# Kernel optimization log

Hardware: AMD Instinct MI355X
Metric: run time of the kernel (lower is better)

## Reference

```python
import jax, jax.numpy as jnp
import numpy as np

N_NODES = 10000
N_EDGES = 160000
NEG_SLOPE = 0.2


def setup_inputs() -> dict:
    key = jax.random.key(0)
    ks = jax.random.split(key, 24)

    def rn(k, shape, scale):
        return (jax.random.normal(k, shape, dtype=jnp.float32) * scale)

    inp = {
        "x": rn(ks[0], (N_NODES, 128), 1.0),
        "edge_index": jax.random.randint(ks[1], (2, N_EDGES), 0, N_NODES, dtype=jnp.int32),
        "edge_attr": rn(ks[2], (N_EDGES, 8), 1.0),
        # GATConv 1: 128 -> 64 (heads=1)
        "W1": rn(ks[3], (128, 64), 0.09), "as1": rn(ks[4], (64,), 0.1), "ad1": rn(ks[5], (64,), 0.1), "b1": rn(ks[6], (64,), 0.01),
        # GATConv 2: 64 -> 256
        "W2": rn(ks[7], (64, 256), 0.125), "as2": rn(ks[8], (256,), 0.06), "ad2": rn(ks[9], (256,), 0.06), "b2": rn(ks[10], (256,), 0.01),
        # GATConv 3: 256 -> 1024
        "W3": rn(ks[11], (256, 1024), 0.0625), "as3": rn(ks[12], (1024,), 0.03), "ad3": rn(ks[13], (1024,), 0.03), "b3": rn(ks[14], (1024,), 0.01),
        # Dense head
        "lw1": rn(ks[15], (1024, 512), 0.03), "lb1": rn(ks[16], (512,), 0.01),
        "lw2": rn(ks[17], (512, 10), 0.04), "lb2": rn(ks[18], (10,), 0.01),
    }
    return inp


def gat_layer(x, src, dst, W, a_s, a_d, b, n):
    """PyG GATConv, heads=1, concat=True, add_self_loops handled by caller via src/dst."""
    h = x @ W                                   # [N, F_out]
    e = jax.nn.leaky_relu((h @ a_s)[src] + (h @ a_d)[dst], NEG_SLOPE)  # [E']
    m = jax.ops.segment_max(e, dst, num_segments=n)
    ex = jnp.exp(e - m[dst])
    denom = jax.ops.segment_sum(ex, dst, num_segments=n)
    alpha = ex / denom[dst]                     # scatter-softmax over incoming edges
    out = jax.ops.segment_sum(alpha[:, None] * h[src], dst, num_segments=n)
    return out + b


def reference(x, edge_index, edge_attr, W1, as1, ad1, b1, W2, as2, ad2, b2,
              W3, as3, ad3, b3, lw1, lb1, lw2, lb2):
    # edge_attr is accepted but ignored (GATConv built without edge_dim)
    n = x.shape[0]
    loops = jnp.arange(n, dtype=edge_index.dtype)  # add_self_loops=True
    src = jnp.concatenate([edge_index[0], loops])
    dst = jnp.concatenate([edge_index[1], loops])

    h = jax.nn.relu(gat_layer(x, src, dst, W1, as1, ad1, b1, n))
    h = jax.nn.relu(gat_layer(h, src, dst, W2, as2, ad2, b2, n))
    h = jax.nn.relu(gat_layer(h, src, dst, W3, as3, ad3, b3, n))

    pooled = jnp.max(h, axis=0, keepdims=True)  # global_max_pool, batch=None -> [1, 1024]
    z = jax.nn.relu(pooled @ lw1 + lb1)
    z = z @ lw2 + lb2
    return jax.nn.log_softmax(z, axis=1)
```

## Files before the change

kernel.cpp:

```cpp
#include <hip/hip_runtime.h>
#include <hip/hip_bf16.h>
#include <math.h>

#define NEG_SLOPE 0.2f
typedef unsigned short u16;
typedef short bf16x8 __attribute__((ext_vector_type(8)));
typedef float f32x4 __attribute__((ext_vector_type(4)));

__device__ __forceinline__ float bfu2f(u16 u) { return __uint_as_float(((unsigned)u) << 16); }
__device__ __forceinline__ u16 f2bu(float v) { return __bfloat16_as_ushort(__float2bfloat16(v)); }

__device__ __forceinline__ void gload_lds16(const void* g, void* l) {
    __builtin_amdgcn_global_load_lds((const __attribute__((address_space(1))) void*)g,
                                     (__attribute__((address_space(3))) void*)l, 16, 0, 0);
}

__global__ void prep_kernel(int* deg, int* cursor, float* pooled, int N,
                            const float* __restrict__ x, u16* __restrict__ xb,
                            const float* __restrict__ W1, u16* __restrict__ Wt1,
                            const float* __restrict__ W2, u16* __restrict__ Wt2,
                            const float* __restrict__ W3, u16* __restrict__ Wt3,
                            const float* __restrict__ as2, const float* __restrict__ ad2,
                            const float* __restrict__ as3, const float* __restrict__ ad3,
                            float* __restrict__ ws2, float* __restrict__ wd2,
                            float* __restrict__ ws3, float* __restrict__ wd3,
                            int c0, int c1, int c2, int c3, int c4) {
    int bid = blockIdx.x, tid = threadIdx.x;
    if (bid < c0) {
        int i = bid * 256 + tid;
        if (i < N) { deg[i] = 0; cursor[i] = 0; }
        if (i < 1024) pooled[i] = 0.f;
    } else if (bid < c1) {
        int i = (bid - c0) * 256 + tid;
        if (i < N * 128) xb[i] = f2bu(x[i]);
    } else if (bid < c2) {
        int i = (bid - c1) * 256 + tid;
        int k = i % 128, f = i / 128;
        Wt1[i] = f2bu(W1[k * 64 + f]);
    } else if (bid < c3) {
        int i = (bid - c2) * 256 + tid;
        int k = i % 64, f = i / 64;
        Wt2[i] = f2bu(W2[k * 256 + f]);
    } else if (bid < c4) {
        int i = (bid - c3) * 256 + tid;
        int k = i % 256, f = i / 256;
        Wt3[i] = f2bu(W3[(size_t)k * 1024 + f]);
    } else {
        int wv = ((bid - c4) * 256 + tid) >> 6;
        int lane = tid & 63;
        const float *W, *va, *vd; float *os, *od; int F, row;
        if (wv < 64) { W = W2; va = as2; vd = ad2; F = 256; row = wv; os = ws2; od = wd2; }
        else if (wv < 320) { W = W3; va = as3; vd = ad3; F = 1024; row = wv - 64; os = ws3; od = wd3; }
        else return;
        const float* wr = W + (size_t)row * F;
        float ss = 0.f, dd = 0.f;
        for (int f = lane; f < F; f += 64) { float wvv = wr[f]; ss += wvv * va[f]; dd += wvv * vd[f]; }
        for (int off = 32; off; off >>= 1) { ss += __shfl_xor(ss, off); dd += __shfl_xor(dd, off); }
        if (lane == 0) { os[row] = ss; od[row] = dd; }
    }
}

__global__ void count_kernel(const int* __restrict__ edst, int E, int N, int* deg) {
    int i = blockIdx.x * blockDim.x + threadIdx.x;
    int total = E + N;
    if (i >= total) return;
    int dn = (i < E) ? edst[i] : (i - E);
    atomicAdd(&deg[dn], 1);
}

__global__ void scan_kernel(const int* __restrict__ deg, int N, int* __restrict__ offsets) {
    __shared__ int part[257];
    int tid = threadIdx.x;
    int chunk = (N + 255) / 256;
    int begin = tid * chunk;
    int fin = begin + chunk; if (fin > N) fin = N; if (begin > N) begin = N;
    int sum = 0;
    for (int i = begin; i < fin; ++i) sum += deg[i];
    part[tid] = sum;
    __syncthreads();
    if (tid == 0) {
        int acc = 0;
        for (int t = 0; t < 256; ++t) { int v = part[t]; part[t] = acc; acc += v; }
        part[256] = acc;
    }
    __syncthreads();
    int acc = part[tid];
    for (int i = begin; i < fin; ++i) { offsets[i] = acc; acc += deg[i]; }
    if (tid == 255) offsets[N] = part[256];
}

__global__ void scatter_kernel(const int* __restrict__ esrc, const int* __restrict__ edst,
                               int E, int N, const int* __restrict__ offsets,
                               int* cursor, int* __restrict__ srcg) {
    int i = blockIdx.x * blockDim.x + threadIdx.x;
    int total = E + N;
    if (i >= total) return;
    int sn, dn;
    if (i < E) { sn = esrc[i]; dn = edst[i]; } else { sn = i - E; dn = i - E; }
    int pos = atomicAdd(&cursor[dn], 1);
    srcg[offsets[dn] + pos] = sn;
}

template <int K, int MR, bool BIASRELU, bool SD_EPI>
__global__ __launch_bounds__(256) void mfma_gemm(const u16* __restrict__ A,
                                                 const u16* __restrict__ Wt,
                                                 u16* __restrict__ C,
                                                 const float* __restrict__ bias,
                                                 int M, int F,
                                                 const float* __restrict__ asv,
                                                 const float* __restrict__ adv,
                                                 float* __restrict__ s_out,
                                                 float* __restrict__ d_out) {
    constexpr int NK = K / 32;
    int tid = threadIdx.x;
    int w = tid >> 6, l = tid & 63;
    int l15 = l & 15, q = l >> 4;
    int bm = blockIdx.x * (64 * MR);
    int bn = blockIdx.y * 64;
    int r0 = bm + w * (16 * MR);

    const u16* aptr[MR];
    int row[MR];
#pragma unroll
    for (int mr = 0; mr < MR; ++mr) {
        int r = r0 + mr * 16 + l15;
        row[mr] = r;
        int ar = (r < M) ? r : (M - 1);
        aptr[mr] = A + (size_t)ar * K + 8 * q;
    }
    const u16* bptr[4];
#pragma unroll
    for (int nt = 0; nt < 4; ++nt)
        bptr[nt] = Wt + (size_t)(bn + nt * 16 + l15) * K + 8 * q;

    f32x4 acc[MR][4];
#pragma unroll
    for (int mr = 0; mr < MR; ++mr)
#pragma unroll
        for (int nt = 0; nt < 4; ++nt) acc[mr][nt] = (f32x4){0.f, 0.f, 0.f, 0.f};

    bf16x8 a_cur[MR], b_cur[4], a_nxt[MR], b_nxt[4];
#pragma unroll
    for (int mr = 0; mr < MR; ++mr) a_cur[mr] = *(const bf16x8*)(aptr[mr]);
#pragma unroll
    for (int nt = 0; nt < 4; ++nt) b_cur[nt] = *(const bf16x8*)(bptr[nt]);

#pragma unroll
    for (int kk = 0; kk < NK; ++kk) {
        if (kk + 1 < NK) {
            int koff = (kk + 1) * 32;
#pragma unroll
            for (int mr = 0; mr < MR; ++mr) a_nxt[mr] = *(const bf16x8*)(aptr[mr] + koff);
#pragma unroll
            for (int nt = 0; nt < 4; ++nt) b_nxt[nt] = *(const bf16x8*)(bptr[nt] + koff);
        }
#pragma unroll
        for (int mr = 0; mr < MR; ++mr)
#pragma unroll
            for (int nt = 0; nt < 4; ++nt)
                acc[mr][nt] = __builtin_amdgcn_mfma_f32_16x16x32_bf16(b_cur[nt], a_cur[mr], acc[mr][nt], 0, 0, 0);
        if (kk + 1 < NK) {
#pragma unroll
            for (int mr = 0; mr < MR; ++mr) a_cur[mr] = a_nxt[mr];
#pragma unroll
            for (int nt = 0; nt < 4; ++nt) b_cur[nt] = b_nxt[nt];
        }
    }

#pragma unroll
    for (int mr = 0; mr < MR; ++mr) {
        if (row[mr] >= M) continue;
#pragma unroll
        for (int nt = 0; nt < 4; ++nt) {
            int col = bn + nt * 16 + 4 * q;
            ushort4 st;
#pragma unroll
            for (int r = 0; r < 4; ++r) {
                float v = acc[mr][nt][r];
                if (BIASRELU) { v += bias[col + r]; v = fmaxf(v, 0.f); }
                ((u16*)&st)[r] = f2bu(v);
            }
            *(ushort4*)(C + (size_t)row[mr] * F + col) = st;
        }
    }

    if constexpr (SD_EPI) {
        float ss = 0.f, dd = 0.f;
#pragma unroll
        for (int nt = 0; nt < 4; ++nt)
#pragma unroll
            for (int r = 0; r < 4; ++r) {
                int col = nt * 16 + 4 * q + r;
                float v = acc[0][nt][r];
                ss += v * asv[col];
                dd += v * adv[col];
            }
        ss += __shfl_xor(ss, 16); ss += __shfl_xor(ss, 32);
        dd += __shfl_xor(dd, 16); dd += __shfl_xor(dd, 32);
        if (q == 0 && row[0] < M) { s_out[row[0]] = ss; d_out[row[0]] = dd; }
    }
}

__global__ __launch_bounds__(512) void gemm3_kernel(const u16* __restrict__ A,
                                                    const u16* __restrict__ Wt,
                                                    const float* __restrict__ bias,
                                                    int M,
                                                    float* __restrict__ pmaxbuf) {
    constexpr int K = 256;
    constexpr int ABYTES = 128 * 512;
    __shared__ char lds[2 * ABYTES];
    int tid = threadIdx.x;
    int w = tid >> 6, lane = tid & 63;
    int w2 = w >> 2, wc = w & 3;
    int l15 = lane & 15, q = lane >> 4;
    int bid = blockIdx.x;
    int rb = bid >> 3, cb = bid & 7;
    int bm = rb * 128, bn = cb * 128;

#pragma unroll
    for (int it = 0; it < 8; ++it) {
        int c = it * 512 + tid;
        int row = c >> 5, kc = c & 31;
        int arow = bm + row; if (arow >= M) arow = M - 1;
        gload_lds16(A + (size_t)arow * K + ((kc ^ (row & 7)) * 8),
                    lds + (size_t)(it * 512 + (tid & ~63)) * 16);
    }
#pragma unroll
    for (int it = 0; it < 8; ++it) {
        int c = it * 512 + tid;
        int col = c >> 5, kc = c & 31;
        gload_lds16(Wt + (size_t)(bn + col) * K + ((kc ^ (col & 7)) * 8),
                    lds + ABYTES + (size_t)(it * 512 + (tid & ~63)) * 16);
    }
    __syncthreads();

    f32x4 acc[4][2];
#pragma unroll
    for (int mr = 0; mr < 4; ++mr)
#pragma unroll
        for (int nt = 0; nt < 2; ++nt) acc[mr][nt] = (f32x4){0.f, 0.f, 0.f, 0.f};

    const char* abase = lds;
    const char* bbase = lds + ABYTES;
#pragma unroll
    for (int kk = 0; kk < 8; ++kk) {
        int c = kk * 4 + q;
        bf16x8 af[4], bfr[2];
#pragma unroll
        for (int mr = 0; mr < 4; ++mr) {
            int row = w2 * 64 + mr * 16 + l15;
            af[mr] = *(const bf16x8*)(abase + row * 512 + ((c ^ (row & 7)) * 16));
        }
#pragma unroll
        for (int nt = 0; nt < 2; ++nt) {
            int col = wc * 32 + nt * 16 + l15;
            bfr[nt] = *(const bf16x8*)(bbase + col * 512 + ((c ^ (col & 7)) * 16));
        }
#pragma unroll
        for (int mr = 0; mr < 4; ++mr)
#pragma unroll
            for (int nt = 0; nt < 2; ++nt)
                acc[mr][nt] = __builtin_amdgcn_mfma_f32_16x16x32_bf16(bfr[nt], af[mr], acc[mr][nt], 0, 0, 0);
    }

    float pmax[2][4];
#pragma unroll
    for (int nt = 0; nt < 2; ++nt)
#pragma unroll
        for (int r = 0; r < 4; ++r) pmax[nt][r] = 0.f;
#pragma unroll
    for (int mr = 0; mr < 4; ++mr) {
        bool valid = (bm + w2 * 64 + mr * 16 + l15) < M;
#pragma unroll
        for (int nt = 0; nt < 2; ++nt)
#pragma unroll
            for (int r = 0; r < 4; ++r) {
                float v = acc[mr][nt][r] + bias[bn + wc * 32 + nt * 16 + 4 * q + r];
                v = fmaxf(v, 0.f);
                if (valid) pmax[nt][r] = fmaxf(pmax[nt][r], v);
            }
    }
#pragma unroll
    for (int nt = 0; nt < 2; ++nt)
#pragma unroll
        for (int r = 0; r < 4; ++r) {
#pragma unroll
            for (int msk = 1; msk < 16; msk <<= 1)
                pmax[nt][r] = fmaxf(pmax[nt][r], __shfl_xor(pmax[nt][r], msk));
        }
    if (l15 == 0) {
#pragma unroll
        for (int nt = 0; nt < 2; ++nt)
#pragma unroll
            for (int r = 0; r < 4; ++r)
                pmaxbuf[(size_t)(rb * 2 + w2) * 1024 + bn + wc * 32 + nt * 16 + 4 * q + r] = pmax[nt][r];
    }
}

__global__ void pool_reduce_kernel(const float* __restrict__ pmaxbuf, int nslices,
                                   float* __restrict__ pooled) {
    int f = blockIdx.x * 256 + threadIdx.x;
    float m = 0.f;
    for (int s = 0; s < nslices; ++s) m = fmaxf(m, pmaxbuf[(size_t)s * 1024 + f]);
    pooled[f] = m;
}

__global__ void sd_kernel(const u16* __restrict__ h, const float* __restrict__ a_s,
                          const float* __restrict__ a_d, int N, int F,
                          float* __restrict__ s, float* __restrict__ d) {
    int wave = (blockIdx.x * blockDim.x + threadIdx.x) >> 6;
    int lane = threadIdx.x & 63;
    if (wave >= N) return;
    const u16* hrow = h + (size_t)wave * F;
    float ss = 0.f, dd = 0.f;
    for (int f = lane * 4; f < F; f += 256) {
        ushort4 u = *reinterpret_cast<const ushort4*>(hrow + f);
        float4 av = *reinterpret_cast<const float4*>(a_s + f);
        float4 dv = *reinterpret_cast<const float4*>(a_d + f);
        float h0 = bfu2f(u.x), h1 = bfu2f(u.y), h2 = bfu2f(u.z), h3 = bfu2f(u.w);
        ss += h0 * av.x + h1 * av.y + h2 * av.z + h3 * av.w;
        dd += h0 * dv.x + h1 * dv.y + h2 * dv.z + h3 * dv.w;
    }
    for (int off = 32; off; off >>= 1) { ss += __shfl_xor(ss, off); dd += __shfl_xor(dd, off); }
    if (lane == 0) { s[wave] = ss; d[wave] = dd; }
}

template <int F, int FS, bool BIASRELU, bool SD_EPI>
__global__ __launch_bounds__(256) void agg_kernel(const u16* __restrict__ h,
                                                  const float* __restrict__ sv,
                                                  const float* __restrict__ dvec,
                                                  const int* __restrict__ srcg,
                                                  const int* __restrict__ offsets,
                                                  const float* __restrict__ bias,
                                                  u16* __restrict__ out,
                                                  const float* __restrict__ wsv,
                                                  const float* __restrict__ wdv,
                                                  float* __restrict__ s_out,
                                                  float* __restrict__ d_out) {
    constexpr int FB = F / FS;
    constexpr int VPT = FB / 64;
    __shared__ float pL[256];
    __shared__ int sL[256];
    __shared__ float red[3][FB];
    int n = blockIdx.x;
    int f0 = blockIdx.y * FB;
    int tid = threadIdx.x;
    int w = tid >> 6, lane = tid & 63;
    int start = offsets[n], end = offsets[n + 1];
    int deg = end - start;
    float dval = dvec[n];
    float acc[VPT];
#pragma unroll
    for (int v = 0; v < VPT; ++v) acc[v] = 0.f;
    float inv;

    auto gpoint = [&](int sn) { return h + (size_t)sn * F + f0 + lane * VPT; };
    auto accum = [&](float pw, const u16* hp) {
        if constexpr (VPT == 4) {
            ushort4 u = *(const ushort4*)hp;
            acc[0] += pw * bfu2f(u.x); acc[1] += pw * bfu2f(u.y);
            acc[2] += pw * bfu2f(u.z); acc[3] += pw * bfu2f(u.w);
        } else if constexpr (VPT == 2) {
            ushort2 u = *(const ushort2*)hp;
            acc[0] += pw * bfu2f(u.x); acc[1] += pw * bfu2f(u.y);
        } else {
            acc[0] += pw * bfu2f(*hp);
        }
    };

    if (deg <= 256) {
        float e = -INFINITY;
        if (tid < deg) {
            int sn = srcg[start + tid];
            sL[tid] = sn;
            float v = sv[sn] + dval;
            e = (v >= 0.f) ? v : NEG_SLOPE * v;
        }
        pL[tid] = e;
        __syncthreads();
        float m = fmaxf(fmaxf(pL[lane], pL[lane + 64]), fmaxf(pL[lane + 128], pL[lane + 192]));
#pragma unroll
        for (int off2 = 32; off2; off2 >>= 1) m = fmaxf(m, __shfl_xor(m, off2));
        __syncthreads();
        float p = (tid < deg) ? expf(e - m) : 0.f;
        pL[tid] = p;
        __syncthreads();
        float t4 = (pL[lane] + pL[lane + 64]) + (pL[lane + 128] + pL[lane + 192]);
#pragma unroll
        for (int off2 = 32; off2; off2 >>= 1) t4 += __shfl_xor(t4, off2);
        inv = 1.f / t4;
        int jj = w;
        for (; jj + 4 < deg; jj += 8) {
            float p0 = pL[jj], p1 = pL[jj + 4];
            const u16* h0 = gpoint(sL[jj]);
            const u16* h1 = gpoint(sL[jj + 4]);
            accum(p0, h0);
            accum(p1, h1);
        }
        if (jj < deg) accum(pL[jj], gpoint(sL[jj]));
    } else {
        float lmax = -INFINITY;
        for (int j = start + lane; j < end; j += 64) {
            float v = sv[srcg[j]] + dval; v = (v >= 0.f) ? v : NEG_SLOPE * v;
            lmax = fmaxf(lmax, v);
        }
#pragma unroll
        for (int off2 = 32; off2; off2 >>= 1) lmax = fmaxf(lmax, __shfl_xor(lmax, off2));
        float ls = 0.f;
        for (int j = start + lane; j < end; j += 64) {
            float v = sv[srcg[j]] + dval; v = (v >= 0.f) ? v : NEG_SLOPE * v;
            ls += expf(v - lmax);
        }
#pragma unroll
        for (int off2 = 32; off2; off2 >>= 1) ls += __shfl_xor(ls, off2);
        inv = 1.f / ls;
        for (int j = start + w; j < end; j += 4) {
            int sn = srcg[j];
            float e2 = sv[sn] + dval; e2 = (e2 >= 0.f) ? e2 : NEG_SLOPE * e2;
            accum(expf(e2 - lmax), gpoint(sn));
        }
    }

    if (w > 0) {
#pragma unroll
        for (int v = 0; v < VPT; ++v) red[w - 1][lane * VPT + v] = acc[v];
    }
    __syncthreads();
    if (w != 0) return;
    float res0 = 0.f;
    if constexpr (VPT == 2) {
        ushort2 st;
#pragma unroll
        for (int v = 0; v < VPT; ++v) {
            float xv = (acc[v] + red[0][lane * 2 + v] + red[1][lane * 2 + v] + red[2][lane * 2 + v]) * inv;
            if (BIASRELU) { xv += bias[f0 + lane * 2 + v]; xv = fmaxf(xv, 0.f); }
            ((u16*)&st)[v] = f2bu(xv);
        }
        *(ushort2*)(out + (size_t)n * F + f0 + lane * 2) = st;
    } else if constexpr (VPT == 1) {
        float xv = (acc[0] + red[0][lane] + red[1][lane] + red[2][lane]) * inv;
        if (BIASRELU) { xv += bias[f0 + lane]; xv = fmaxf(xv, 0.f); }
        res0 = xv;
        out[(size_t)n * F + f0 + lane] = f2bu(xv);
    } else {
        ushort4 st;
#pragma unroll
        for (int v = 0; v < VPT; ++v) {
            float xv = (acc[v] + red[0][lane * 4 + v] + red[1][lane * 4 + v] + red[2][lane * 4 + v]) * inv;
            if (BIASRELU) { xv += bias[f0 + lane * 4 + v]; xv = fmaxf(xv, 0.f); }
            ((u16*)&st)[v] = f2bu(xv);
        }
        *(ushort4*)(out + (size_t)n * F + f0 + lane * 4) = st;
    }
    if constexpr (SD_EPI) {
        float ss = res0 * wsv[lane], dd = res0 * wdv[lane];
        for (int off2 = 32; off2; off2 >>= 1) { ss += __shfl_xor(ss, off2); dd += __shfl_xor(dd, off2); }
        if (lane == 0) { s_out[n] = ss; d_out[n] = dd; }
    }
}

__global__ void head1a_kernel(const float* __restrict__ pooled, const float* __restrict__ lw1,
                              float* __restrict__ part) {
    int j = blockIdx.x * 128 + threadIdx.x;
    int k0 = blockIdx.y * 64;
    float acc = 0.f;
#pragma unroll 8
    for (int k = k0; k < k0 + 64; ++k) acc += pooled[k] * lw1[(size_t)k * 512 + j];
    part[blockIdx.y * 512 + j] = acc;
}

__global__ void head1bc_kernel(const float* __restrict__ part, const float* __restrict__ lb1,
                               const float* __restrict__ lw2, const float* __restrict__ lb2,
                               float* __restrict__ out) {
    __shared__ float zs[512];
    __shared__ float z2s[10];
    int tid = threadIdx.x;
    if (tid < 512) {
        float acc = lb1[tid];
#pragma unroll
        for (int t = 0; t < 16; ++t) acc += part[t * 512 + tid];
        zs[tid] = fmaxf(acc, 0.f);
    }
    __syncthreads();
    int w = tid >> 6, lane = tid & 63;
    if (w < 10) {
        float acc = 0.f;
#pragma unroll
        for (int kc = 0; kc < 8; ++kc) {
            int k = kc * 64 + lane;
            acc += zs[k] * lw2[k * 10 + w];
        }
        for (int off = 32; off; off >>= 1) acc += __shfl_xor(acc, off);
        if (lane == 0) z2s[w] = acc + lb2[w];
    }
    __syncthreads();
    if (tid == 0) {
        float m = z2s[0];
        for (int j = 1; j < 10; ++j) m = fmaxf(m, z2s[j]);
        float ssum = 0.f;
        for (int j = 0; j < 10; ++j) ssum += expf(z2s[j] - m);
        float lse = m + logf(ssum);
        for (int j = 0; j < 10; ++j) out[j] = z2s[j] - lse;
    }
}

extern "C" void kernel_launch(void* const* d_in, const int* in_sizes, int n_in,
                              void* d_out, int out_size, void* d_ws, size_t ws_size,
                              hipStream_t stream) {
    const float* x   = (const float*)d_in[0];
    const int* ei    = (const int*)d_in[1];
    const float* W1  = (const float*)d_in[3];
    const float* as1 = (const float*)d_in[4];
    const float* ad1 = (const float*)d_in[5];
    const float* b1  = (const float*)d_in[6];
    const float* W2  = (const float*)d_in[7];
    const float* as2 = (const float*)d_in[8];
    const float* ad2 = (const float*)d_in[9];
    const float* b2  = (const float*)d_in[10];
    const float* W3  = (const float*)d_in[11];
    const float* as3 = (const float*)d_in[12];
    const float* ad3 = (const float*)d_in[13];
    const float* b3  = (const float*)d_in[14];
    const float* lw1 = (const float*)d_in[15];
    const float* lb1 = (const float*)d_in[16];
    const float* lw2 = (const float*)d_in[17];
    const float* lb2 = (const float*)d_in[18];
    float* out = (float*)d_out;

    const int N = in_sizes[0] / 128;
    const int E = in_sizes[1] / 2;
    const int total = E + N;
    const int* esrc = ei;
    const int* edst = ei + E;

    char* base = (char*)d_ws;
    size_t off = 0;
    auto alloc = [&](size_t bytes) { void* p = base + off; off = (off + bytes + 255) & ~(size_t)255; return p; };
    u16* xb    = (u16*)alloc((size_t)N * 128 * 2);
    u16* h1    = (u16*)alloc((size_t)N * 64 * 2);
    u16* a1    = (u16*)alloc((size_t)N * 64 * 2);
    u16* agg2b = (u16*)alloc((size_t)N * 64 * 2);
    u16* a2    = (u16*)alloc((size_t)N * 256 * 2);
    u16* agg3b = (u16*)alloc((size_t)N * 256 * 2);
    u16* Wt1   = (u16*)alloc(128 * 64 * 2);
    u16* Wt2   = (u16*)alloc(64 * 256 * 2);
    u16* Wt3   = (u16*)alloc(256 * 1024 * 2);
    float* ws2 = (float*)alloc(64 * 4);
    float* wd2 = (float*)alloc(64 * 4);
    float* ws3 = (float*)alloc(256 * 4);
    float* wd3 = (float*)alloc(256 * 4);
    float* sbuf = (float*)alloc((size_t)N * 4);
    float* dbuf = (float*)alloc((size_t)N * 4);
    float* pooled = (float*)alloc(1024 * 4);
    float* hpart  = (float*)alloc(16 * 512 * 4);
    int* deg     = (int*)alloc((size_t)N * 4);
    int* cursor  = (int*)alloc((size_t)N * 4);
    int* offsets = (int*)alloc((size_t)(N + 1) * 4);
    int* srcg    = (int*)alloc((size_t)total * 4);
    int nrb128g = (N + 127) / 128;
    float* pmaxbuf = (float*)alloc((size_t)nrb128g * 2 * 1024 * 4);

    const int TPB = 256;
    int gE = (total + TPB - 1) / TPB;
    int gW = (N + 3) / 4;
    int gR64 = (N + 63) / 64;
    int gR128 = (N + 127) / 128;

    int c0 = (N + 255) / 256;
    int c1 = c0 + (N * 128 + 255) / 256;
    int c2 = c1 + (128 * 64) / 256;
    int c3 = c2 + (64 * 256) / 256;
    int c4 = c3 + (256 * 1024) / 256;
    int gP = c4 + 80;
    prep_kernel<<<gP, TPB, 0, stream>>>(deg, cursor, pooled, N, x, xb,
                                        W1, Wt1, W2, Wt2, W3, Wt3,
                                        as2, ad2, as3, ad3, ws2, wd2, ws3, wd3,
                                        c0, c1, c2, c3, c4);

    count_kernel<<<gE, TPB, 0, stream>>>(edst, E, N, deg);
    scan_kernel<<<1, TPB, 0, stream>>>(deg, N, offsets);
    scatter_kernel<<<gE, TPB, 0, stream>>>(esrc, edst, E, N, offsets, cursor, srcg);

    mfma_gemm<128, 1, false, true><<<dim3(gR64, 1), TPB, 0, stream>>>(
        xb, Wt1, h1, nullptr, N, 64, as1, ad1, sbuf, dbuf);
    agg_kernel<64, 1, true, true><<<dim3(N, 1), TPB, 0, stream>>>(
        h1, sbuf, dbuf, srcg, offsets, b1, a1, ws2, wd2, sbuf, dbuf);

    agg_kernel<64, 1, false, false><<<dim3(N, 1), TPB, 0, stream>>>(
        a1, sbuf, dbuf, srcg, offsets, nullptr, agg2b, nullptr, nullptr, nullptr, nullptr);
    mfma_gemm<64, 2, true, false><<<dim3(gR128, 4), TPB, 0, stream>>>(
        agg2b, Wt2, a2, b2, N, 256, nullptr, nullptr, nullptr, nullptr);

    sd_kernel<<<gW, TPB, 0, stream>>>(a2, ws3, wd3, N, 256, sbuf, dbuf);
    agg_kernel<256, 2, false, false><<<dim3(N, 2), TPB, 0, stream>>>(
        a2, sbuf, dbuf, srcg, offsets, nullptr, agg3b, nullptr, nullptr, nullptr, nullptr);
    gemm3_kernel<<<nrb128g * 8, 512, 0, stream>>>(agg3b, Wt3, b3, N, pmaxbuf);
    pool_reduce_kernel<<<4, TPB, 0, stream>>>(pmaxbuf, nrb128g * 2, pooled);

    head1a_kernel<<<dim3(4, 16), 128, 0, stream>>>(pooled, lw1, hpart);
    head1bc_kernel<<<1, 640, 0, stream>>>(hpart, lb1, lw2, lb2, out);
}
```

Baseline: 193.1 us.

## Reuse A tile across two column blocks in gemm3, fuse pool reduce into head

Each gemm3 block now loads its 128-row A tile once and loops over two 128-column halves of Wt3, halving the block count and the redundant A loads. The separate pool_reduce kernel is removed, and the max over slices is folded into the first head kernel through a shared-memory staging step. The layer-3 aggregation launch also changes from 2 to 4 column splits per node. In exchange, each gemm3 block does its two halves one after the other with an extra barrier, so there are fewer blocks to spread across the GPU.

```diff
diff --git a/kernel.cpp b/kernel.cpp
--- a/kernel.cpp
+++ b/kernel.cpp
@@ -214,8 +214,8 @@
     int w2 = w >> 2, wc = w & 3;
     int l15 = lane & 15, q = lane >> 4;
     int bid = blockIdx.x;
-    int rb = bid >> 3, cb = bid & 7;
-    int bm = rb * 128, bn = cb * 128;
+    int rb = bid >> 2, cbp = bid & 3;
+    int bm = rb * 128;
 
 #pragma unroll
     for (int it = 0; it < 8; ++it) {
@@ -225,84 +225,83 @@
         gload_lds16(A + (size_t)arow * K + ((kc ^ (row & 7)) * 8),
                     lds + (size_t)(it * 512 + (tid & ~63)) * 16);
     }
-#pragma unroll
-    for (int it = 0; it < 8; ++it) {
-        int c = it * 512 + tid;
-        int col = c >> 5, kc = c & 31;
-        gload_lds16(Wt + (size_t)(bn + col) * K + ((kc ^ (col & 7)) * 8),
-                    lds + ABYTES + (size_t)(it * 512 + (tid & ~63)) * 16);
-    }
-    __syncthreads();
-
-    f32x4 acc[4][2];
-#pragma unroll
-    for (int mr = 0; mr < 4; ++mr)
-#pragma unroll
-        for (int nt = 0; nt < 2; ++nt) acc[mr][nt] = (f32x4){0.f, 0.f, 0.f, 0.f};
 
     const char* abase = lds;
-    const char* bbase = lds + ABYTES;
-#pragma unroll
-    for (int kk = 0; kk < 8; ++kk) {
-        int c = kk * 4 + q;
-        bf16x8 af[4], bfr[2];
+    char* bldst = lds + ABYTES;
+
+    for (int half = 0; half < 2; ++half) {
+        if (half) __syncthreads();
+        int bn = cbp * 256 + half * 128;
+#pragma unroll
+        for (int it = 0; it < 8; ++it) {
+            int c = it * 512 + tid;
+            int col = c >> 5, kc = c & 31;
+            gload_lds16(Wt + (size_t)(bn + col) * K + ((kc ^ (col & 7)) * 8),
+                        bldst + (size_t)(it * 512 + (tid & ~63)) * 16);
+        }
+        __syncthreads();
+
+        f32x4 acc[4][2];
+#pragma unroll
+        for (int mr = 0; mr < 4; ++mr)
+#pragma unroll
+            for (int nt = 0; nt < 2; ++nt) acc[mr][nt] = (f32x4){0.f, 0.f, 0.f, 0.f};
+
+        const char* bbase = bldst;
+#pragma unroll
+        for (int kk = 0; kk < 8; ++kk) {
+            int c = kk * 4 + q;
+            bf16x8 af[4], bfr[2];
+#pragma unroll
+            for (int mr = 0; mr < 4; ++mr) {
+                int row = w2 * 64 + mr * 16 + l15;
+                af[mr] = *(const bf16x8*)(abase + row * 512 + ((c ^ (row & 7)) * 16));
+            }
+#pragma unroll
+            for (int nt = 0; nt < 2; ++nt) {
+                int col = wc * 32 + nt * 16 + l15;
+                bfr[nt] = *(const bf16x8*)(bbase + col * 512 + ((c ^ (col & 7)) * 16));
+            }
+#pragma unroll
+            for (int mr = 0; mr < 4; ++mr)
+#pragma unroll
+                for (int nt = 0; nt < 2; ++nt)
+                    acc[mr][nt] = __builtin_amdgcn_mfma_f32_16x16x32_bf16(bfr[nt], af[mr], acc[mr][nt], 0, 0, 0);
+        }
+
+        float pmax[2][4];
+#pragma unroll
+        for (int nt = 0; nt < 2; ++nt)
+#pragma unroll
+            for (int r = 0; r < 4; ++r) pmax[nt][r] = 0.f;
 #pragma unroll
         for (int mr = 0; mr < 4; ++mr) {
-            int row = w2 * 64 + mr * 16 + l15;
-            af[mr] = *(const bf16x8*)(abase + row * 512 + ((c ^ (row & 7)) * 16));
-        }
-#pragma unroll
-        for (int nt = 0; nt < 2; ++nt) {
-            int col = wc * 32 + nt * 16 + l15;
-            bfr[nt] = *(const bf16x8*)(bbase + col * 512 + ((c ^ (col & 7)) * 16));
-        }
-#pragma unroll
-        for (int mr = 0; mr < 4; ++mr)
+            bool valid = (bm + w2 * 64 + mr * 16 + l15) < M;
 #pragma unroll
             for (int nt = 0; nt < 2; ++nt)
-                acc[mr][nt] = __builtin_amdgcn_mfma_f32_16x16x32_bf16(bfr[nt], af[mr], acc[mr][nt], 0, 0, 0);
-    }
-
-    float pmax[2][4];
-#pragma unroll
-    for (int nt = 0; nt < 2; ++nt)
-#pragma unroll
-        for (int r = 0; r < 4; ++r) pmax[nt][r] = 0.f;
-#pragma unroll
-    for (int mr = 0; mr < 4; ++mr) {
-        bool valid = (bm + w2 * 64 + mr * 16 + l15) < M;
+#pragma unroll
+                for (int r = 0; r < 4; ++r) {
+                    float v = acc[mr][nt][r] + bias[bn + wc * 32 + nt * 16 + 4 * q + r];
+                    v = fmaxf(v, 0.f);
+                    if (valid) pmax[nt][r] = fmaxf(pmax[nt][r], v);
+                }
+        }
 #pragma unroll
         for (int nt = 0; nt < 2; ++nt)
 #pragma unroll
             for (int r = 0; r < 4; ++r) {
-                float v = acc[mr][nt][r] + bias[bn + wc * 32 + nt * 16 + 4 * q + r];
-                v = fmaxf(v, 0.f);
-                if (valid) pmax[nt][r] = fmaxf(pmax[nt][r], v);
+#pragma unroll
+                for (int msk = 1; msk < 16; msk <<= 1)
+                    pmax[nt][r] = fmaxf(pmax[nt][r], __shfl_xor(pmax[nt][r], msk));
             }
-    }
-#pragma unroll
-    for (int nt = 0; nt < 2; ++nt)
-#pragma unroll
-        for (int r = 0; r < 4; ++r) {
-#pragma unroll
-            for (int msk = 1; msk < 16; msk <<= 1)
-                pmax[nt][r] = fmaxf(pmax[nt][r], __shfl_xor(pmax[nt][r], msk));
-        }
-    if (l15 == 0) {
-#pragma unroll
-        for (int nt = 0; nt < 2; ++nt)
-#pragma unroll
-            for (int r = 0; r < 4; ++r)
-                pmaxbuf[(size_t)(rb * 2 + w2) * 1024 + bn + wc * 32 + nt * 16 + 4 * q + r] = pmax[nt][r];
-    }
-}
-
-__global__ void pool_reduce_kernel(const float* __restrict__ pmaxbuf, int nslices,
-                                   float* __restrict__ pooled) {
-    int f = blockIdx.x * 256 + threadIdx.x;
-    float m = 0.f;
-    for (int s = 0; s < nslices; ++s) m = fmaxf(m, pmaxbuf[(size_t)s * 1024 + f]);
-    pooled[f] = m;
+        if (l15 == 0) {
+#pragma unroll
+            for (int nt = 0; nt < 2; ++nt)
+#pragma unroll
+                for (int r = 0; r < 4; ++r)
+                    pmaxbuf[(size_t)(rb * 2 + w2) * 1024 + bn + wc * 32 + nt * 16 + 4 * q + r] = pmax[nt][r];
+        }
+    }
 }
 
 __global__ void sd_kernel(const u16* __restrict__ h, const float* __restrict__ a_s,
@@ -459,13 +458,22 @@
     }
 }
 
-__global__ void head1a_kernel(const float* __restrict__ pooled, const float* __restrict__ lw1,
-                              float* __restrict__ part) {
-    int j = blockIdx.x * 128 + threadIdx.x;
+__global__ void head1ap_kernel(const float* __restrict__ pmaxbuf, int nslices,
+                               const float* __restrict__ lw1, float* __restrict__ part) {
+    __shared__ float pk[64];
+    int tid = threadIdx.x;
     int k0 = blockIdx.y * 64;
+    if (tid < 64) {
+        float m = 0.f;
+#pragma unroll 4
+        for (int s = 0; s < nslices; ++s) m = fmaxf(m, pmaxbuf[(size_t)s * 1024 + k0 + tid]);
+        pk[tid] = m;
+    }
+    __syncthreads();
+    int j = blockIdx.x * 128 + tid;
     float acc = 0.f;
 #pragma unroll 8
-    for (int k = k0; k < k0 + 64; ++k) acc += pooled[k] * lw1[(size_t)k * 512 + j];
+    for (int kk = 0; kk < 64; ++kk) acc += pk[kk] * lw1[(size_t)(k0 + kk) * 512 + j];
     part[blockIdx.y * 512 + j] = acc;
 }
 
@@ -592,11 +600,10 @@
         agg2b, Wt2, a2, b2, N, 256, nullptr, nullptr, nullptr, nullptr);
 
     sd_kernel<<<gW, TPB, 0, stream>>>(a2, ws3, wd3, N, 256, sbuf, dbuf);
-    agg_kernel<256, 2, false, false><<<dim3(N, 2), TPB, 0, stream>>>(
+    agg_kernel<256, 4, false, false><<<dim3(N, 4), TPB, 0, stream>>>(
         a2, sbuf, dbuf, srcg, offsets, nullptr, agg3b, nullptr, nullptr, nullptr, nullptr);
-    gemm3_kernel<<<nrb128g * 8, 512, 0, stream>>>(agg3b, Wt3, b3, N, pmaxbuf);
-    pool_reduce_kernel<<<4, TPB, 0, stream>>>(pmaxbuf, nrb128g * 2, pooled);
-
-    head1a_kernel<<<dim3(4, 16), 128, 0, stream>>>(pooled, lw1, hpart);
+    gemm3_kernel<<<nrb128g * 4, 512, 0, stream>>>(agg3b, Wt3, b3, N, pmaxbuf);
+
+    head1ap_kernel<<<dim3(4, 16), 128, 0, stream>>>(pmaxbuf, nrb128g * 2, lw1, hpart);
     head1bc_kernel<<<1, 640, 0, stream>>>(hpart, lb1, lw2, lb2, out);
 }
```

After: 217.6 us. +12.7%, slower.
